# Kernel tuning notes

Hardware: AMD Instinct MI355X
Metric: run time of the kernel (lower is better)

The kernel has to match this reference:

```python
import jax, jax.numpy as jnp
import numpy as np

C = 6      # in_channel (forced by the module's own shape constraints)
MID = 3    # in_channel // 2
EPS = 1e-5


def setup_inputs() -> dict:
    key = jax.random.key(0)
    ks = jax.random.split(key, 16)
    B, N, NC, L = 2, 32768, 3, 2048
    w = lambda k, shape: jax.random.normal(k, shape, jnp.float32) * 0.2
    return {
        "x": jax.random.normal(ks[0], (B, C, N), jnp.float32),
        "curves": jax.random.normal(ks[1], (B, C, NC, L), jnp.float32),
        "Wa": w(ks[2], (MID, C)),    # conva   (Conv1d C->MID, k=1, no bias)
        "Wav": w(ks[3], (MID, C)),   # conva_v
        "Wb": w(ks[4], (MID, C)),    # convb
        "Wbv": w(ks[5], (MID, C)),   # convb_v
        "Wc": w(ks[6], (MID, C)),    # convc
        "Wd": w(ks[7], (C, 2 * MID)),  # convd Conv1d 2*MID -> C
        "bn_gamma": jnp.ones((C,), jnp.float32),
        "bn_beta": jnp.zeros((C,), jnp.float32),
        "Watt": w(ks[8], (C,)),      # line_conv_att Conv2d C->1, k=1
        "ln_gamma": jnp.ones((2 * MID,), jnp.float32),
        "ln_beta": jnp.zeros((2 * MID,), jnp.float32),
        "Wpl": w(ks[9], (MID, 3)),   # p_l Conv1d 3->MID (with bias)
        "bpl": w(ks[10], (MID,)),
        "Wpn": w(ks[11], (MID, 3)),  # p_n Conv1d 3->MID (with bias)
        "bpn": w(ks[12], (MID,)),
    }


def reference(x, curves, Wa, Wav, Wb, Wbv, Wc, Wd, bn_gamma, bn_beta,
              Watt, ln_gamma, ln_beta, Wpl, bpl, Wpn, bpn):
    # p, curve = curves  (tensor unpack along dim 0)
    p = curves[0]                                        # [C, 3, L]
    # p_l / p_n: Conv1d(3, MID) with p treated as batch=C, channels=3
    pl = jnp.einsum('bkl,mk->bml', p, Wpl) + bpl[None, :, None]   # [C, MID, L]
    p_l = pl.mean(axis=-1)                               # [C, MID]
    pn = jnp.einsum('bkl,mk->bml', p, Wpn) + bpn[None, :, None]   # [C, MID, L]
    p_n = pn.mean(axis=-2)                               # [C, L]

    # line attention over curves
    att = jnp.einsum('bcnl,c->bnl', curves, Watt)[:, None, :, :]  # [B,1,3,L]
    curver_inter = (curves * jax.nn.softmax(att, axis=-1)).sum(axis=-1)  # [B,C,3]
    curves_intra = (curves * jax.nn.softmax(att, axis=-2)).sum(axis=-2)  # [B,C,L]

    gi = curver_inter + p_l                              # [B,C,3] + [C,3(MID)]
    ga = curves_intra + p_n                              # [B,C,L] + [C,L]
    k_inter = jnp.einsum('bcn,mc->bmn', gi, Wa)          # [B,MID,3]
    v_inter = jnp.einsum('bcn,mc->bnm', gi, Wav)         # [B,3,MID]
    k_intra = jnp.einsum('bcl,mc->bml', ga, Wb)          # [B,MID,L]
    v_intra = jnp.einsum('bcl,mc->blm', ga, Wbv)         # [B,L,MID]

    q = jnp.einsum('bcn,mc->bnm', x, Wc)                 # [B,N,MID]
    scale = jnp.sqrt(jnp.float32(q.shape[-1]))           # sqrt(MID)

    att_inter = jax.nn.softmax(jnp.einsum('bnm,bmk->bnk', q, k_inter) / scale, axis=-1)
    feature_inter = jnp.einsum('bnk,bkm->bnm', att_inter, v_inter)   # [B,N,MID]
    att_intra = jax.nn.softmax(jnp.einsum('bnm,bml->bnl', q, k_intra) / scale, axis=-1)
    feature_intra = jnp.einsum('bnl,blm->bnm', att_intra, v_intra)   # [B,N,MID]

    cf = jnp.concatenate([feature_inter, feature_intra], axis=-1)    # [B,N,2*MID]
    mu = cf.mean(axis=-1, keepdims=True)
    var = ((cf - mu) ** 2).mean(axis=-1, keepdims=True)
    cf = (cf - mu) * jax.lax.rsqrt(var + EPS) * ln_gamma + ln_beta   # LayerNorm
    cf = jnp.swapaxes(cf, 1, 2)                                      # [B,2*MID,N]

    y = jnp.einsum('bcn,oc->bon', cf, Wd)                # Conv1d 2*MID -> C
    # BatchNorm1d (training-mode batch statistics over (B, N))
    bm = y.mean(axis=(0, 2), keepdims=True)
    bv = ((y - bm) ** 2).mean(axis=(0, 2), keepdims=True)
    y = (y - bm) * jax.lax.rsqrt(bv + EPS) * bn_gamma[None, :, None] + bn_beta[None, :, None]

    out = x + y
    return jnp.where(out >= 0, out, 0.2 * out)           # LeakyReLU(0.2)
```

## Files before the change

kernel.cpp:

```cpp
#include <hip/hip_runtime.h>
#include <math.h>

#define N_PTS 32768
#define LL    2048

#define KT_U      0
#define VT_U      8192
#define PART_OFF  16384
#define MS_OFF    28672
#define W_OFF     28684
#define CS_OFF    28720
#define PBKM_OFF  28738
#define BNS_OFF   28762
#define BNB_OFF   28768

typedef __fp16 h2    __attribute__((ext_vector_type(2)));
typedef __fp16 f16x4 __attribute__((ext_vector_type(4)));
typedef float  f32x4 __attribute__((ext_vector_type(4)));

__device__ __forceinline__ unsigned h2_bits(h2 h){
  union { h2 h; unsigned u; } x; x.h = h; return x.u;
}
__device__ __forceinline__ float wave_reduce_sum(float v){
  #pragma unroll
  for (int off = 32; off; off >>= 1) v += __shfl_xor(v, off, 64);
  return v;
}
__device__ __forceinline__ float wave_reduce_max(float v){
  #pragma unroll
  for (int off = 32; off; off >>= 1) v = fmaxf(v, __shfl_xor(v, off, 64));
  return v;
}

__global__ __launch_bounds__(256)
void prep_kernel(const float* __restrict__ curves, const float* __restrict__ Watt,
                 const float* __restrict__ Wb,  const float* __restrict__ Wbv,
                 const float* __restrict__ Wpn, const float* __restrict__ bpn,
                 float* __restrict__ ws)
{
  const int blk = blockIdx.x, tid = threadIdx.x;
  const int lane = tid & 63, wid = tid >> 6;
  __shared__ float sred[4 * 13];
  __shared__ float msh;

  float watt[6];
  #pragma unroll
  for (int c = 0; c < 6; c++) watt[c] = Watt[c];

  if (blk < 6) {
    const int b = blk / 3, nc = blk % 3;
    const float* cb = curves + b * 18 * LL;
    float av[8], pm = -1e30f;
    #pragma unroll
    for (int k = 0; k < 8; k++) {
      const int l = tid + k * 256;
      float s = 0.f;
      #pragma unroll
      for (int c = 0; c < 6; c++) s = fmaf(cb[(c * 3 + nc) * LL + l], watt[c], s);
      av[k] = s; pm = fmaxf(pm, s);
    }
    pm = wave_reduce_max(pm);
    if (lane == 0) sred[wid] = pm;
    __syncthreads();
    if (tid == 0) msh = fmaxf(fmaxf(sred[0], sred[1]), fmaxf(sred[2], sred[3]));
    __syncthreads();
    const float m = msh;

    float vals[13];
    #pragma unroll
    for (int j = 0; j < 13; j++) vals[j] = 0.f;
    #pragma unroll
    for (int k = 0; k < 8; k++) {
      const int l = tid + k * 256;
      float e = __expf(av[k] - m);
      vals[0] += e;
      #pragma unroll
      for (int c = 0; c < 6; c++) {
        float v = cb[(c * 3 + nc) * LL + l];
        vals[1 + c] = fmaf(v, e, vals[1 + c]);
        if (b == 0) vals[7 + c] += v;
      }
    }
    __syncthreads();
    #pragma unroll
    for (int j = 0; j < 13; j++) vals[j] = wave_reduce_sum(vals[j]);
    if (lane == 0) { for (int j = 0; j < 13; j++) sred[wid * 13 + j] = vals[j]; }
    __syncthreads();
    if (tid == 0) {
      ws[MS_OFF + blk * 2] = m;
      for (int j = 0; j < 13; j++) {
        float s = sred[j] + sred[13 + j] + sred[26 + j] + sred[39 + j];
        if (j == 0) ws[MS_OFF + blk * 2 + 1] = s;
        else if (j < 7) ws[W_OFF + blk * 6 + (j - 1)] = s;
        else if (b == 0) ws[CS_OFF + nc * 6 + (j - 7)] = s;
      }
    }
  } else {
    const int idx = (blk - 6) * 256 + tid;
    const int b = idx >> 10, pp = idx & 1023, l = pp * 2;
    const float* cb = curves + b * 18 * LL;

    float2 cv[6][3], pv[6][3];
    #pragma unroll
    for (int c = 0; c < 6; c++)
      #pragma unroll
      for (int nc = 0; nc < 3; nc++) {
        cv[c][nc] = *(const float2*)&cb[(c * 3 + nc) * LL + l];
        pv[c][nc] = *(const float2*)&curves[(c * 3 + nc) * LL + l];
      }
    float a[3][2];
    #pragma unroll
    for (int nc = 0; nc < 3; nc++) {
      float sx = 0.f, sy = 0.f;
      #pragma unroll
      for (int c = 0; c < 6; c++) {
        sx = fmaf(cv[c][nc].x, watt[c], sx);
        sy = fmaf(cv[c][nc].y, watt[c], sy);
      }
      a[nc][0] = sx; a[nc][1] = sy;
    }

    float wb_r[18], wbv_r[18];
    #pragma unroll
    for (int i = 0; i < 18; i++) { wb_r[i] = Wb[i]; wbv_r[i] = Wbv[i]; }
    const float wn0 = (Wpn[0] + Wpn[3] + Wpn[6]) * (1.f / 3.f);
    const float wn1 = (Wpn[1] + Wpn[4] + Wpn[7]) * (1.f / 3.f);
    const float wn2 = (Wpn[2] + Wpn[5] + Wpn[8]) * (1.f / 3.f);
    const float bnb = (bpn[0] + bpn[1] + bpn[2]) * (1.f / 3.f);

    float kk[2][3], vv[2][3], km[3] = {0.f, 0.f, 0.f};
    #pragma unroll
    for (int e = 0; e < 2; e++) {
      float a0 = a[0][e], a1 = a[1][e], a2 = a[2][e];
      float mm = fmaxf(fmaxf(a0, a1), a2);
      float e0 = __expf(a0 - mm), e1 = __expf(a1 - mm), e2 = __expf(a2 - mm);
      float r = 1.f / (e0 + e1 + e2);
      float ga[6];
      #pragma unroll
      for (int c = 0; c < 6; c++) {
        float c0 = e ? cv[c][0].y : cv[c][0].x;
        float c1 = e ? cv[c][1].y : cv[c][1].x;
        float c2 = e ? cv[c][2].y : cv[c][2].x;
        float p0 = e ? pv[c][0].y : pv[c][0].x;
        float p1 = e ? pv[c][1].y : pv[c][1].x;
        float p2 = e ? pv[c][2].y : pv[c][2].x;
        float intra = (c0 * e0 + c1 * e1 + c2 * e2) * r;
        float pn = p0 * wn0 + p1 * wn1 + p2 * wn2 + bnb;
        ga[c] = intra + pn;
      }
      float k0 = 0, k1 = 0, k2 = 0, v0 = 0, v1 = 0, v2 = 0;
      #pragma unroll
      for (int c = 0; c < 6; c++) {
        k0 += wb_r[c] * ga[c];  k1 += wb_r[6 + c] * ga[c];  k2 += wb_r[12 + c] * ga[c];
        v0 += wbv_r[c] * ga[c]; v1 += wbv_r[6 + c] * ga[c]; v2 += wbv_r[12 + c] * ga[c];
      }
      kk[e][0] = k0; kk[e][1] = k1; kk[e][2] = k2;
      vv[e][0] = v0; vv[e][1] = v1; vv[e][2] = v2;
      km[0] = fmaxf(km[0], fabsf(k0));
      km[1] = fmaxf(km[1], fabsf(k1));
      km[2] = fmaxf(km[2], fabsf(k2));
    }

    unsigned* ktg = (unsigned*)ws + KT_U + b * 4096;
    #pragma unroll
    for (int e = 0; e < 2; e++) {
      const int k = l + e;
      const int idxk = (k >> 5) * 64 + (k & 15) * 4 + (((k >> 4) & 1) << 1);
      ktg[idxk]     = h2_bits(__builtin_amdgcn_cvt_pkrtz(kk[e][0], kk[e][1]));
      ktg[idxk + 1] = h2_bits(__builtin_amdgcn_cvt_pkrtz(kk[e][2], 0.f));
    }
    {
      unsigned* vtg = (unsigned*)ws + VT_U + b * 4096;
      const int cp = pp >> 4, c2 = (pp >> 3) & 1, p = (2 * pp) & 15;
      const int base = cp * 64 + (p >> 2) * 4 + c2 * 2 + ((p >> 1) & 1);
      vtg[base]      = h2_bits(__builtin_amdgcn_cvt_pkrtz(vv[0][0], vv[1][0]));
      vtg[base + 16] = h2_bits(__builtin_amdgcn_cvt_pkrtz(vv[0][1], vv[1][1]));
      vtg[base + 32] = h2_bits(__builtin_amdgcn_cvt_pkrtz(vv[0][2], vv[1][2]));
      vtg[base + 48] = h2_bits(__builtin_amdgcn_cvt_pkrtz(1.f, 1.f));
    }

    #pragma unroll
    for (int j = 0; j < 3; j++) km[j] = wave_reduce_max(km[j]);
    if (lane == 0) { for (int j = 0; j < 3; j++) sred[wid * 3 + j] = km[j]; }
    __syncthreads();
    if (tid == 0) {
      for (int j = 0; j < 3; j++)
        ws[PBKM_OFF + (blk - 6) * 3 + j] =
          fmaxf(fmaxf(sred[j], sred[3 + j]), fmaxf(sred[6 + j], sred[9 + j]));
    }
  }
}

__global__ __launch_bounds__(1024, 4)
void attn_kernel(const float* __restrict__ x,  const float* __restrict__ Wc,
                 const float* __restrict__ Wd, const float* __restrict__ lng,
                 const float* __restrict__ lnb,
                 const float* __restrict__ Wa, const float* __restrict__ Wav,
                 const float* __restrict__ Wpl, const float* __restrict__ bpl,
                 float* __restrict__ ws, float* __restrict__ yout)
{
  __shared__ __align__(16) unsigned kt[4224];
  __shared__ __align__(16) unsigned vt[4224];
  __shared__ float4 cross[4][2][64];
  __shared__ float cp[16 * 12];
  __shared__ float gis[18], kis[9], vis[9];
  const int tid  = threadIdx.x, blk = blockIdx.x;
  const int lane = tid & 63, w = tid >> 6;
  const int col  = lane & 15, hi4 = lane >> 4;
  const int rg   = w >> 2, rp = (w >> 1) & 1, kh = w & 1;
  const int rbase = blk * 256;
  const int b    = rbase >> 15;
  const int nb   = rbase & (N_PTS - 1);

  {
    const uint4* ktg = (const uint4*)((const unsigned*)ws + KT_U + b * 4096);
    const uint4* vtg = (const uint4*)((const unsigned*)ws + VT_U + b * 4096);
    ((uint4*)kt)[tid] = ktg[tid];
    ((uint4*)vt)[tid] = vtg[tid];
    if (tid < 8) { kt[4096 + tid] = 0; vt[4096 + tid] = 0; }
  }
  if (tid < 18) {
    int c = tid / 3, m = tid % 3;
    float pl_ = bpl[m];
    #pragma unroll
    for (int k = 0; k < 3; k++)
      pl_ = fmaf(Wpl[m * 3 + k], ws[CS_OFF + k * 6 + c] * (1.f / LL), pl_);
    gis[c * 3 + m] = ws[W_OFF + (b * 3 + m) * 6 + c] / ws[MS_OFF + (b * 3 + m) * 2 + 1] + pl_;
  }
  __syncthreads();
  if (tid < 9) {
    int m = tid / 3, k = tid % 3;
    float s1 = 0.f, s2 = 0.f;
    #pragma unroll
    for (int c = 0; c < 6; c++) {
      float g = gis[c * 3 + k];
      s1 = fmaf(Wa [m * 6 + c], g, s1);
      s2 = fmaf(Wav[m * 6 + c], g, s2);
    }
    kis[m * 3 + k] = s1; vis[k * 3 + m] = s2;
  }

  float km0 = 0.f, km1 = 0.f, km2 = 0.f;
  #pragma unroll
  for (int s = 0; s < 4; s++) {
    const float* pk = ws + PBKM_OFF + (b * 4 + s) * 3;
    km0 = fmaxf(km0, pk[0]); km1 = fmaxf(km1, pk[1]); km2 = fmaxf(km2, pk[2]);
  }

  const int nA = nb + rg * 64 + rp * 32 + col, nBr = nA + 16;
  const float* xb = x + (size_t)b * 6 * N_PTS;
  float q0A = 0, q1A = 0, q2A = 0, q0B = 0, q1B = 0, q2B = 0;
  #pragma unroll
  for (int c = 0; c < 6; c++) {
    float xvA = xb[c * N_PTS + nA], xvB = xb[c * N_PTS + nBr];
    q0A = fmaf(xvA, Wc[c], q0A); q1A = fmaf(xvA, Wc[6 + c], q1A); q2A = fmaf(xvA, Wc[12 + c], q2A);
    q0B = fmaf(xvB, Wc[c], q0B); q1B = fmaf(xvB, Wc[6 + c], q1B); q2B = fmaf(xvB, Wc[12 + c], q2B);
  }
  const float KS = 1.4426950408889634f * 0.57735026918962576f;
  q0A *= KS; q1A *= KS; q2A *= KS; q0B *= KS; q1B *= KS; q2B *= KS;
  const float MpA = fabsf(q0A) * km0 + fabsf(q1A) * km1 + fabsf(q2A) * km2;
  const float MpB = fabsf(q0B) * km0 + fabsf(q1B) * km1 + fabsf(q2B) * km2;

  union U2 { uint2 u; f16x4 h; };
  union U4 { uint4 q; f16x4 h[2]; };
  U2 qbA, qbB;
  qbA.u.x = qbA.u.y = qbB.u.x = qbB.u.y = 0;
  if (hi4 == 0) {
    qbA.u.x = h2_bits(__builtin_amdgcn_cvt_pkrtz(q0A, q1A));
    qbA.u.y = h2_bits(__builtin_amdgcn_cvt_pkrtz(q2A, 0.f));
    qbB.u.x = h2_bits(__builtin_amdgcn_cvt_pkrtz(q0B, q1B));
    qbB.u.y = h2_bits(__builtin_amdgcn_cvt_pkrtz(q2B, 0.f));
  }
  f32x4 cbA = { -MpA, -MpA, -MpA, -MpA };
  f32x4 cbB = { -MpB, -MpB, -MpB, -MpB };
  f32x4 aA0 = {0,0,0,0}, aA1 = {0,0,0,0}, aB0 = {0,0,0,0}, aB1 = {0,0,0,0};

  unsigned ki_ = (hi4 == 0) ? (unsigned)(kh * 2048 + col * 4) : 4096u;
  const unsigned kd = (hi4 == 0) ? 64u : 0u;
  unsigned vi_ = (col < 4) ? (unsigned)(kh * 2048 + col * 16 + hi4 * 4) : 4096u;
  const unsigned vd = (col < 4) ? 64u : 0u;

  __syncthreads();

  U4 Kc, Vc;
  Kc.q = *(const uint4*)&kt[ki_];
  Vc.q = *(const uint4*)&vt[vi_];

  for (int i = 0; i < 32; i++) {
    ki_ += kd; vi_ += vd;
    U4 Kn, Vn;
    Kn.q = *(const uint4*)&kt[ki_];
    Vn.q = *(const uint4*)&vt[vi_];

    f32x4 s0A = __builtin_amdgcn_mfma_f32_16x16x16f16(Kc.h[0], qbA.h, cbA, 0, 0, 0);
    f32x4 s0B = __builtin_amdgcn_mfma_f32_16x16x16f16(Kc.h[0], qbB.h, cbB, 0, 0, 0);
    f32x4 s1A = __builtin_amdgcn_mfma_f32_16x16x16f16(Kc.h[1], qbA.h, cbA, 0, 0, 0);
    f32x4 s1B = __builtin_amdgcn_mfma_f32_16x16x16f16(Kc.h[1], qbB.h, cbB, 0, 0, 0);

    U2 PA, PB;
    {
      float e0 = __builtin_amdgcn_exp2f(s0A[0]);
      float e1 = __builtin_amdgcn_exp2f(s0A[1]);
      float e2 = __builtin_amdgcn_exp2f(s0A[2]);
      float e3 = __builtin_amdgcn_exp2f(s0A[3]);
      float f0 = __builtin_amdgcn_exp2f(s0B[0]);
      float f1 = __builtin_amdgcn_exp2f(s0B[1]);
      float f2 = __builtin_amdgcn_exp2f(s0B[2]);
      float f3 = __builtin_amdgcn_exp2f(s0B[3]);
      PA.u.x = h2_bits(__builtin_amdgcn_cvt_pkrtz(e0, e1));
      PA.u.y = h2_bits(__builtin_amdgcn_cvt_pkrtz(e2, e3));
      PB.u.x = h2_bits(__builtin_amdgcn_cvt_pkrtz(f0, f1));
      PB.u.y = h2_bits(__builtin_amdgcn_cvt_pkrtz(f2, f3));
    }
    aA0 = __builtin_amdgcn_mfma_f32_16x16x16f16(Vc.h[0], PA.h, aA0, 0, 0, 0);
    aB0 = __builtin_amdgcn_mfma_f32_16x16x16f16(Vc.h[0], PB.h, aB0, 0, 0, 0);
    {
      float e0 = __builtin_amdgcn_exp2f(s1A[0]);
      float e1 = __builtin_amdgcn_exp2f(s1A[1]);
      float e2 = __builtin_amdgcn_exp2f(s1A[2]);
      float e3 = __builtin_amdgcn_exp2f(s1A[3]);
      float f0 = __builtin_amdgcn_exp2f(s1B[0]);
      float f1 = __builtin_amdgcn_exp2f(s1B[1]);
      float f2 = __builtin_amdgcn_exp2f(s1B[2]);
      float f3 = __builtin_amdgcn_exp2f(s1B[3]);
      PA.u.x = h2_bits(__builtin_amdgcn_cvt_pkrtz(e0, e1));
      PA.u.y = h2_bits(__builtin_amdgcn_cvt_pkrtz(e2, e3));
      PB.u.x = h2_bits(__builtin_amdgcn_cvt_pkrtz(f0, f1));
      PB.u.y = h2_bits(__builtin_amdgcn_cvt_pkrtz(f2, f3));
    }
    aA1 = __builtin_amdgcn_mfma_f32_16x16x16f16(Vc.h[1], PA.h, aA1, 0, 0, 0);
    aB1 = __builtin_amdgcn_mfma_f32_16x16x16f16(Vc.h[1], PB.h, aB1, 0, 0, 0);

    Kc = Kn; Vc = Vn;
  }

  if (hi4 == 0) {
    cross[rg][kh][rp * 32 + col] =
      make_float4(aA0[0] + aA1[0], aA0[1] + aA1[1], aA0[2] + aA1[2], aA0[3] + aA1[3]);
    cross[rg][kh][rp * 32 + 16 + col] =
      make_float4(aB0[0] + aB1[0], aB0[1] + aB1[1], aB0[2] + aB1[2], aB0[3] + aB1[3]);
  }
  __syncthreads();

  float v12[12];
  #pragma unroll
  for (int j = 0; j < 12; j++) v12[j] = 0.f;

  if (tid < 256) {
    const int trg = tid >> 6, ri = tid & 63;
    const int n = nb + trg * 64 + ri;
    float4 c0 = cross[trg][0][ri], c1 = cross[trg][1][ri];
    float w0 = c0.x + c1.x, w1 = c0.y + c1.y, w2 = c0.z + c1.z, dd = c0.w + c1.w;

    float a0 = 0, a1 = 0, a2 = 0;
    #pragma unroll
    for (int c = 0; c < 6; c++) {
      float xv = xb[c * N_PTS + n];
      a0 = fmaf(xv, Wc[c], a0); a1 = fmaf(xv, Wc[6 + c], a1); a2 = fmaf(xv, Wc[12 + c], a2);
    }
    a0 *= KS; a1 *= KS; a2 *= KS;

    float sk0 = a0 * kis[0] + a1 * kis[3] + a2 * kis[6];
    float sk1 = a0 * kis[1] + a1 * kis[4] + a2 * kis[7];
    float sk2 = a0 * kis[2] + a1 * kis[5] + a2 * kis[8];
    float mm  = fmaxf(fmaxf(sk0, sk1), sk2);
    float e0 = __builtin_amdgcn_exp2f(sk0 - mm);
    float e1 = __builtin_amdgcn_exp2f(sk1 - mm);
    float e2 = __builtin_amdgcn_exp2f(sk2 - mm);
    float rs = 1.f / (e0 + e1 + e2);
    float fi0 = (e0 * vis[0] + e1 * vis[3] + e2 * vis[6]) * rs;
    float fi1 = (e0 * vis[1] + e1 * vis[4] + e2 * vis[7]) * rs;
    float fi2 = (e0 * vis[2] + e1 * vis[5] + e2 * vis[8]) * rs;
    float rinv = 1.f / dd;
    float cf[6] = { fi0, fi1, fi2, w0 * rinv, w1 * rinv, w2 * rinv };

    float mu = (cf[0] + cf[1] + cf[2] + cf[3] + cf[4] + cf[5]) * (1.f / 6.f);
    float var = 0.f;
    #pragma unroll
    for (int i = 0; i < 6; i++) { float t = cf[i] - mu; var += t * t; }
    var *= (1.f / 6.f);
    float rn = rsqrtf(var + 1e-5f);
    float cfn[6];
    #pragma unroll
    for (int i = 0; i < 6; i++) cfn[i] = (cf[i] - mu) * rn * lng[i] + lnb[i];

    #pragma unroll
    for (int o = 0; o < 6; o++) {
      float s = 0.f;
      #pragma unroll
      for (int c = 0; c < 6; c++) s += Wd[o * 6 + c] * cfn[c];
      yout[(size_t)b * (6 * N_PTS) + o * N_PTS + n] = s;
      v12[o] = s; v12[6 + o] = s * s;
    }
  }

  #pragma unroll
  for (int j = 0; j < 12; j++) v12[j] = wave_reduce_sum(v12[j]);
  if (lane == 0) { for (int j = 0; j < 12; j++) cp[w * 12 + j] = v12[j]; }
  __syncthreads();
  if (tid == 0) {
    float* part = ws + PART_OFF + blk * 12;
    for (int j = 0; j < 12; j++)
      part[j] = cp[j] + cp[12 + j] + cp[24 + j] + cp[36 + j];
  }
}

__global__ __launch_bounds__(256)
void final_kernel(const float* __restrict__ x,
                  const float* __restrict__ bng, const float* __restrict__ bnbt,
                  const float* __restrict__ ws, float* __restrict__ out)
{
  __shared__ float cp[48];
  __shared__ float sc_s[6], sh_s[6];
  const int tid = threadIdx.x, blk = blockIdx.x;
  const int lane = tid & 63, wid = tid >> 6;
  const float* part = ws + PART_OFF;

  float v[12];
  #pragma unroll
  for (int j = 0; j < 12; j++) v[j] = part[tid * 12 + j];
  #pragma unroll
  for (int j = 0; j < 12; j++) v[j] = wave_reduce_sum(v[j]);
  if (lane == 0) { for (int j = 0; j < 12; j++) cp[wid * 12 + j] = v[j]; }
  __syncthreads();
  if (tid < 6) {
    const float inv = 1.f / 65536.f;
    float s1 = cp[tid] + cp[12 + tid] + cp[24 + tid] + cp[36 + tid];
    float s2 = cp[6 + tid] + cp[18 + tid] + cp[30 + tid] + cp[42 + tid];
    float mean = s1 * inv;
    float varr = s2 * inv - mean * mean;
    float sc = bng[tid] * rsqrtf(varr + 1e-5f);
    sc_s[tid] = sc;
    sh_s[tid] = bnbt[tid] - mean * sc;
  }
  __syncthreads();

  const int base = blk * 1024 + tid * 4;
  const int ch = (base >> 15) % 6;
  const float sc = sc_s[ch], sh = sh_s[ch];
  float4 o = *(float4*)&out[base];
  float4 xx = *(const float4*)&x[base];
  float r[4] = { o.x * sc + sh + xx.x, o.y * sc + sh + xx.y,
                 o.z * sc + sh + xx.z, o.w * sc + sh + xx.w };
  #pragma unroll
  for (int j = 0; j < 4; j++) r[j] = r[j] >= 0.f ? r[j] : 0.2f * r[j];
  *(float4*)&out[base] = make_float4(r[0], r[1], r[2], r[3]);
}

extern "C" void kernel_launch(void* const* d_in, const int* in_sizes, int n_in,
                              void* d_out, int out_size, void* d_ws, size_t ws_size,
                              hipStream_t stream)
{
  const float* x      = (const float*)d_in[0];
  const float* curves = (const float*)d_in[1];
  const float* Wa     = (const float*)d_in[2];
  const float* Wav    = (const float*)d_in[3];
  const float* Wb     = (const float*)d_in[4];
  const float* Wbv    = (const float*)d_in[5];
  const float* Wc     = (const float*)d_in[6];
  const float* Wd     = (const float*)d_in[7];
  const float* bng    = (const float*)d_in[8];
  const float* bnbt   = (const float*)d_in[9];
  const float* Watt   = (const float*)d_in[10];
  const float* lng    = (const float*)d_in[11];
  const float* lnbt   = (const float*)d_in[12];
  const float* Wpl    = (const float*)d_in[13];
  const float* bpl    = (const float*)d_in[14];
  const float* Wpn    = (const float*)d_in[15];
  const float* bpn    = (const float*)d_in[16];
  float* out = (float*)d_out;
  float* ws  = (float*)d_ws;

  prep_kernel<<<14, 256, 0, stream>>>(curves, Watt, Wb, Wbv, Wpn, bpn, ws);
  attn_kernel<<<256, 1024, 0, stream>>>(x, Wc, Wd, lng, lnbt,
                                        Wa, Wav, Wpl, bpl, ws, out);
  final_kernel<<<384, 256, 0, stream>>>(x, bng, bnbt, ws, out);
}
```

Baseline: 33.63 us.

## Split prep softmax across more blocks and shrink attn blocks to 64 rows

The prep stage's inter-curve softmax reduction is split across 8 blocks per group. Each block writes a partial max, sum and weighted sum, and the attention kernel merges them with a log-sum-exp rescale. The attention kernel now runs 1024 blocks of 512 threads, each covering 64 rows, with 4-way key splitting across waves. The double-buffered K/V loads and the dual accumulators are dropped, and the final kernel sums four times as many BN partials. The goal is better occupancy and load balance across CUs. The cost is more partial writes, more reloading of K/V tables into LDS per block, and less latency hiding in the inner loop.

```diff
diff --git a/kernel.cpp b/kernel.cpp
--- a/kernel.cpp
+++ b/kernel.cpp
@@ -7,12 +7,10 @@
 #define KT_U      0
 #define VT_U      8192
 #define PART_OFF  16384
-#define MS_OFF    28672
-#define W_OFF     28684
-#define CS_OFF    28720
-#define PBKM_OFF  28738
-#define BNS_OFF   28762
-#define BNB_OFF   28768
+#define MS2_OFF   28672
+#define W2_OFF    28768
+#define CS2_OFF   29056
+#define PBKM_OFF  29200
 
 typedef __fp16 h2    __attribute__((ext_vector_type(2)));
 typedef __fp16 f16x4 __attribute__((ext_vector_type(4)));
@@ -47,19 +45,19 @@
   #pragma unroll
   for (int c = 0; c < 6; c++) watt[c] = Watt[c];
 
-  if (blk < 6) {
-    const int b = blk / 3, nc = blk % 3;
+  if (blk < 48) {
+    const int g = blk >> 3, s = blk & 7;
+    const int b = g / 3, nc = g % 3;
+    const int l = s * 256 + tid;
     const float* cb = curves + b * 18 * LL;
-    float av[8], pm = -1e30f;
-    #pragma unroll
-    for (int k = 0; k < 8; k++) {
-      const int l = tid + k * 256;
-      float s = 0.f;
-      #pragma unroll
-      for (int c = 0; c < 6; c++) s = fmaf(cb[(c * 3 + nc) * LL + l], watt[c], s);
-      av[k] = s; pm = fmaxf(pm, s);
-    }
-    pm = wave_reduce_max(pm);
+
+    float cv[6], av = 0.f;
+    #pragma unroll
+    for (int c = 0; c < 6; c++) {
+      cv[c] = cb[(c * 3 + nc) * LL + l];
+      av = fmaf(cv[c], watt[c], av);
+    }
+    float pm = wave_reduce_max(av);
     if (lane == 0) sred[wid] = pm;
     __syncthreads();
     if (tid == 0) msh = fmaxf(fmaxf(sred[0], sred[1]), fmaxf(sred[2], sred[3]));
@@ -67,19 +65,12 @@
     const float m = msh;
 
     float vals[13];
-    #pragma unroll
-    for (int j = 0; j < 13; j++) vals[j] = 0.f;
-    #pragma unroll
-    for (int k = 0; k < 8; k++) {
-      const int l = tid + k * 256;
-      float e = __expf(av[k] - m);
-      vals[0] += e;
-      #pragma unroll
-      for (int c = 0; c < 6; c++) {
-        float v = cb[(c * 3 + nc) * LL + l];
-        vals[1 + c] = fmaf(v, e, vals[1 + c]);
-        if (b == 0) vals[7 + c] += v;
-      }
+    float e = __expf(av - m);
+    vals[0] = e;
+    #pragma unroll
+    for (int c = 0; c < 6; c++) {
+      vals[1 + c] = cv[c] * e;
+      vals[7 + c] = cv[c];
     }
     __syncthreads();
     #pragma unroll
@@ -87,16 +78,17 @@
     if (lane == 0) { for (int j = 0; j < 13; j++) sred[wid * 13 + j] = vals[j]; }
     __syncthreads();
     if (tid == 0) {
-      ws[MS_OFF + blk * 2] = m;
-      for (int j = 0; j < 13; j++) {
-        float s = sred[j] + sred[13 + j] + sred[26 + j] + sred[39 + j];
-        if (j == 0) ws[MS_OFF + blk * 2 + 1] = s;
-        else if (j < 7) ws[W_OFF + blk * 6 + (j - 1)] = s;
-        else if (b == 0) ws[CS_OFF + nc * 6 + (j - 7)] = s;
-      }
+      float t[13];
+      for (int j = 0; j < 13; j++)
+        t[j] = sred[j] + sred[13 + j] + sred[26 + j] + sred[39 + j];
+      ws[MS2_OFF + (g * 8 + s) * 2]     = m;
+      ws[MS2_OFF + (g * 8 + s) * 2 + 1] = t[0];
+      for (int c = 0; c < 6; c++) ws[W2_OFF + (g * 8 + s) * 6 + c] = t[1 + c];
+      if (b == 0)
+        for (int c = 0; c < 6; c++) ws[CS2_OFF + (nc * 8 + s) * 6 + c] = t[7 + c];
     }
   } else {
-    const int idx = (blk - 6) * 256 + tid;
+    const int idx = (blk - 48) * 256 + tid;
     const int b = idx >> 10, pp = idx & 1023, l = pp * 2;
     const float* cb = curves + b * 18 * LL;
 
@@ -185,13 +177,13 @@
     __syncthreads();
     if (tid == 0) {
       for (int j = 0; j < 3; j++)
-        ws[PBKM_OFF + (blk - 6) * 3 + j] =
+        ws[PBKM_OFF + (blk - 48) * 3 + j] =
           fmaxf(fmaxf(sred[j], sred[3 + j]), fmaxf(sred[6 + j], sred[9 + j]));
     }
   }
 }
 
-__global__ __launch_bounds__(1024, 4)
+__global__ __launch_bounds__(512, 8)
 void attn_kernel(const float* __restrict__ x,  const float* __restrict__ Wc,
                  const float* __restrict__ Wd, const float* __restrict__ lng,
                  const float* __restrict__ lnb,
@@ -199,33 +191,48 @@
                  const float* __restrict__ Wpl, const float* __restrict__ bpl,
                  float* __restrict__ ws, float* __restrict__ yout)
 {
-  __shared__ __align__(16) unsigned kt[4224];
-  __shared__ __align__(16) unsigned vt[4224];
-  __shared__ float4 cross[4][2][64];
-  __shared__ float cp[16 * 12];
+  __shared__ __align__(16) unsigned kt[4104];
+  __shared__ __align__(16) unsigned vt[4104];
+  __shared__ float4 cross[4][4][16];
   __shared__ float gis[18], kis[9], vis[9];
   const int tid  = threadIdx.x, blk = blockIdx.x;
   const int lane = tid & 63, w = tid >> 6;
   const int col  = lane & 15, hi4 = lane >> 4;
-  const int rg   = w >> 2, rp = (w >> 1) & 1, kh = w & 1;
-  const int rbase = blk * 256;
+  const int rp   = w >> 2, kq = w & 3;
+  const int rbase = blk * 64;
   const int b    = rbase >> 15;
   const int nb   = rbase & (N_PTS - 1);
 
   {
     const uint4* ktg = (const uint4*)((const unsigned*)ws + KT_U + b * 4096);
     const uint4* vtg = (const uint4*)((const unsigned*)ws + VT_U + b * 4096);
-    ((uint4*)kt)[tid] = ktg[tid];
-    ((uint4*)vt)[tid] = vtg[tid];
+    uint4* kt4 = (uint4*)kt;
+    uint4* vt4 = (uint4*)vt;
+    for (int i = tid; i < 1024; i += 512) { kt4[i] = ktg[i]; vt4[i] = vtg[i]; }
     if (tid < 8) { kt[4096 + tid] = 0; vt[4096 + tid] = 0; }
   }
   if (tid < 18) {
-    int c = tid / 3, m = tid % 3;
+    const int c = tid / 3, m = tid % 3;
+    const int g = b * 3 + m;
+    float mx = -1e30f;
+    #pragma unroll
+    for (int s = 0; s < 8; s++) mx = fmaxf(mx, ws[MS2_OFF + (g * 8 + s) * 2]);
+    float sum = 0.f, Wc_ = 0.f;
+    #pragma unroll
+    for (int s = 0; s < 8; s++) {
+      float e = __expf(ws[MS2_OFF + (g * 8 + s) * 2] - mx);
+      sum += ws[MS2_OFF + (g * 8 + s) * 2 + 1] * e;
+      Wc_ += ws[W2_OFF + (g * 8 + s) * 6 + c] * e;
+    }
     float pl_ = bpl[m];
     #pragma unroll
-    for (int k = 0; k < 3; k++)
-      pl_ = fmaf(Wpl[m * 3 + k], ws[CS_OFF + k * 6 + c] * (1.f / LL), pl_);
-    gis[c * 3 + m] = ws[W_OFF + (b * 3 + m) * 6 + c] / ws[MS_OFF + (b * 3 + m) * 2 + 1] + pl_;
+    for (int k = 0; k < 3; k++) {
+      float cs = 0.f;
+      #pragma unroll
+      for (int s = 0; s < 8; s++) cs += ws[CS2_OFF + (k * 8 + s) * 6 + c];
+      pl_ = fmaf(Wpl[m * 3 + k], cs * (1.f / LL), pl_);
+    }
+    gis[c * 3 + m] = Wc_ / sum + pl_;
   }
   __syncthreads();
   if (tid < 9) {
@@ -247,12 +254,12 @@
     km0 = fmaxf(km0, pk[0]); km1 = fmaxf(km1, pk[1]); km2 = fmaxf(km2, pk[2]);
   }
 
-  const int nA = nb + rg * 64 + rp * 32 + col, nBr = nA + 16;
+  const int nA = nb + rp * 32 + col;
   const float* xb = x + (size_t)b * 6 * N_PTS;
   float q0A = 0, q1A = 0, q2A = 0, q0B = 0, q1B = 0, q2B = 0;
   #pragma unroll
   for (int c = 0; c < 6; c++) {
-    float xvA = xb[c * N_PTS + nA], xvB = xb[c * N_PTS + nBr];
+    float xvA = xb[c * N_PTS + nA], xvB = xb[c * N_PTS + nA + 16];
     q0A = fmaf(xvA, Wc[c], q0A); q1A = fmaf(xvA, Wc[6 + c], q1A); q2A = fmaf(xvA, Wc[12 + c], q2A);
     q0B = fmaf(xvB, Wc[c], q0B); q1B = fmaf(xvB, Wc[6 + c], q1B); q2B = fmaf(xvB, Wc[12 + c], q2B);
   }
@@ -273,29 +280,25 @@
   }
   f32x4 cbA = { -MpA, -MpA, -MpA, -MpA };
   f32x4 cbB = { -MpB, -MpB, -MpB, -MpB };
-  f32x4 aA0 = {0,0,0,0}, aA1 = {0,0,0,0}, aB0 = {0,0,0,0}, aB1 = {0,0,0,0};
-
-  unsigned ki_ = (hi4 == 0) ? (unsigned)(kh * 2048 + col * 4) : 4096u;
+  f32x4 aA = {0,0,0,0}, aB = {0,0,0,0};
+
+  unsigned ki_ = (hi4 == 0) ? (unsigned)(kq * 1024 + col * 4) : 4096u;
   const unsigned kd = (hi4 == 0) ? 64u : 0u;
-  unsigned vi_ = (col < 4) ? (unsigned)(kh * 2048 + col * 16 + hi4 * 4) : 4096u;
+  unsigned vi_ = (col < 4) ? (unsigned)(kq * 1024 + col * 16 + hi4 * 4) : 4096u;
   const unsigned vd = (col < 4) ? 64u : 0u;
 
   __syncthreads();
 
-  U4 Kc, Vc;
-  Kc.q = *(const uint4*)&kt[ki_];
-  Vc.q = *(const uint4*)&vt[vi_];
-
-  for (int i = 0; i < 32; i++) {
+  for (int i = 0; i < 16; i++) {
+    U4 K, V;
+    K.q = *(const uint4*)&kt[ki_];
+    V.q = *(const uint4*)&vt[vi_];
     ki_ += kd; vi_ += vd;
-    U4 Kn, Vn;
-    Kn.q = *(const uint4*)&kt[ki_];
-    Vn.q = *(const uint4*)&vt[vi_];
-
-    f32x4 s0A = __builtin_amdgcn_mfma_f32_16x16x16f16(Kc.h[0], qbA.h, cbA, 0, 0, 0);
-    f32x4 s0B = __builtin_amdgcn_mfma_f32_16x16x16f16(Kc.h[0], qbB.h, cbB, 0, 0, 0);
-    f32x4 s1A = __builtin_amdgcn_mfma_f32_16x16x16f16(Kc.h[1], qbA.h, cbA, 0, 0, 0);
-    f32x4 s1B = __builtin_amdgcn_mfma_f32_16x16x16f16(Kc.h[1], qbB.h, cbB, 0, 0, 0);
+
+    f32x4 s0A = __builtin_amdgcn_mfma_f32_16x16x16f16(K.h[0], qbA.h, cbA, 0, 0, 0);
+    f32x4 s0B = __builtin_amdgcn_mfma_f32_16x16x16f16(K.h[0], qbB.h, cbB, 0, 0, 0);
+    f32x4 s1A = __builtin_amdgcn_mfma_f32_16x16x16f16(K.h[1], qbA.h, cbA, 0, 0, 0);
+    f32x4 s1B = __builtin_amdgcn_mfma_f32_16x16x16f16(K.h[1], qbB.h, cbB, 0, 0, 0);
 
     U2 PA, PB;
     {
@@ -312,8 +315,8 @@
       PB.u.x = h2_bits(__builtin_amdgcn_cvt_pkrtz(f0, f1));
       PB.u.y = h2_bits(__builtin_amdgcn_cvt_pkrtz(f2, f3));
     }
-    aA0 = __builtin_amdgcn_mfma_f32_16x16x16f16(Vc.h[0], PA.h, aA0, 0, 0, 0);
-    aB0 = __builtin_amdgcn_mfma_f32_16x16x16f16(Vc.h[0], PB.h, aB0, 0, 0, 0);
+    aA = __builtin_amdgcn_mfma_f32_16x16x16f16(V.h[0], PA.h, aA, 0, 0, 0);
+    aB = __builtin_amdgcn_mfma_f32_16x16x16f16(V.h[0], PB.h, aB, 0, 0, 0);
     {
       float e0 = __builtin_amdgcn_exp2f(s1A[0]);
       float e1 = __builtin_amdgcn_exp2f(s1A[1]);
@@ -328,29 +331,25 @@
       PB.u.x = h2_bits(__builtin_amdgcn_cvt_pkrtz(f0, f1));
       PB.u.y = h2_bits(__builtin_amdgcn_cvt_pkrtz(f2, f3));
     }
-    aA1 = __builtin_amdgcn_mfma_f32_16x16x16f16(Vc.h[1], PA.h, aA1, 0, 0, 0);
-    aB1 = __builtin_amdgcn_mfma_f32_16x16x16f16(Vc.h[1], PB.h, aB1, 0, 0, 0);
-
-    Kc = Kn; Vc = Vn;
+    aA = __builtin_amdgcn_mfma_f32_16x16x16f16(V.h[1], PA.h, aA, 0, 0, 0);
+    aB = __builtin_amdgcn_mfma_f32_16x16x16f16(V.h[1], PB.h, aB, 0, 0, 0);
   }
 
   if (hi4 == 0) {
-    cross[rg][kh][rp * 32 + col] =
-      make_float4(aA0[0] + aA1[0], aA0[1] + aA1[1], aA0[2] + aA1[2], aA0[3] + aA1[3]);
-    cross[rg][kh][rp * 32 + 16 + col] =
-      make_float4(aB0[0] + aB1[0], aB0[1] + aB1[1], aB0[2] + aB1[2], aB0[3] + aB1[3]);
+    cross[rp * 2][kq][col]     = make_float4(aA[0], aA[1], aA[2], aA[3]);
+    cross[rp * 2 + 1][kq][col] = make_float4(aB[0], aB[1], aB[2], aB[3]);
   }
   __syncthreads();
 
-  float v12[12];
-  #pragma unroll
-  for (int j = 0; j < 12; j++) v12[j] = 0.f;
-
-  if (tid < 256) {
-    const int trg = tid >> 6, ri = tid & 63;
-    const int n = nb + trg * 64 + ri;
-    float4 c0 = cross[trg][0][ri], c1 = cross[trg][1][ri];
-    float w0 = c0.x + c1.x, w1 = c0.y + c1.y, w2 = c0.z + c1.z, dd = c0.w + c1.w;
+  if (tid < 64) {
+    const int rt = tid >> 4, ri = tid & 15;
+    const int n = nb + tid;
+    float4 c0 = cross[rt][0][ri], c1 = cross[rt][1][ri];
+    float4 c2 = cross[rt][2][ri], c3 = cross[rt][3][ri];
+    float w0 = c0.x + c1.x + c2.x + c3.x;
+    float w1 = c0.y + c1.y + c2.y + c3.y;
+    float w2 = c0.z + c1.z + c2.z + c3.z;
+    float dd = c0.w + c1.w + c2.w + c3.w;
 
     float a0 = 0, a1 = 0, a2 = 0;
     #pragma unroll
@@ -384,6 +383,7 @@
     #pragma unroll
     for (int i = 0; i < 6; i++) cfn[i] = (cf[i] - mu) * rn * lng[i] + lnb[i];
 
+    float v12[12];
     #pragma unroll
     for (int o = 0; o < 6; o++) {
       float s = 0.f;
@@ -392,16 +392,12 @@
       yout[(size_t)b * (6 * N_PTS) + o * N_PTS + n] = s;
       v12[o] = s; v12[6 + o] = s * s;
     }
-  }
-
-  #pragma unroll
-  for (int j = 0; j < 12; j++) v12[j] = wave_reduce_sum(v12[j]);
-  if (lane == 0) { for (int j = 0; j < 12; j++) cp[w * 12 + j] = v12[j]; }
-  __syncthreads();
-  if (tid == 0) {
-    float* part = ws + PART_OFF + blk * 12;
-    for (int j = 0; j < 12; j++)
-      part[j] = cp[j] + cp[12 + j] + cp[24 + j] + cp[36 + j];
+    #pragma unroll
+    for (int j = 0; j < 12; j++) v12[j] = wave_reduce_sum(v12[j]);
+    if (tid == 0) {
+      float* part = ws + PART_OFF + blk * 12;
+      for (int j = 0; j < 12; j++) part[j] = v12[j];
+    }
   }
 }
 
@@ -418,7 +414,13 @@
 
   float v[12];
   #pragma unroll
-  for (int j = 0; j < 12; j++) v[j] = part[tid * 12 + j];
+  for (int j = 0; j < 12; j++) v[j] = 0.f;
+  #pragma unroll
+  for (int k = 0; k < 4; k++) {
+    const float* p = part + (tid * 4 + k) * 12;
+    #pragma unroll
+    for (int j = 0; j < 12; j++) v[j] += p[j];
+  }
   #pragma unroll
   for (int j = 0; j < 12; j++) v[j] = wave_reduce_sum(v[j]);
   if (lane == 0) { for (int j = 0; j < 12; j++) cp[wid * 12 + j] = v[j]; }
@@ -471,8 +473,8 @@
   float* out = (float*)d_out;
   float* ws  = (float*)d_ws;
 
-  prep_kernel<<<14, 256, 0, stream>>>(curves, Watt, Wb, Wbv, Wpn, bpn, ws);
-  attn_kernel<<<256, 1024, 0, stream>>>(x, Wc, Wd, lng, lnbt,
+  prep_kernel<<<56, 256, 0, stream>>>(curves, Watt, Wb, Wbv, Wpn, bpn, ws);
+  attn_kernel<<<1024, 512, 0, stream>>>(x, Wc, Wd, lng, lnbt,
                                         Wa, Wav, Wpl, bpl, ws, out);
   final_kernel<<<384, 256, 0, stream>>>(x, bng, bnbt, ws, out);
 }
```

New measurement: 33.50 us, median of 2. About the same (-0.4%).
